# Performance work log

Hardware: AMD Instinct MI355X
Metric: run time of the kernel (lower is better)

## Reference

```python
import jax, jax.numpy as jnp
import numpy as np

L_IMG, L_TXT, B, C, T, D = 12, 12, 64, 1000, 8, 512


def setup_inputs() -> dict:
    key = jax.random.key(0)
    ks = jax.random.split(key, 8)
    s = 0.05  # keep attention logits in a sane range
    return {
        "x": jax.random.normal(ks[0], (L_IMG, B, D), jnp.float32),                 # per-layer projected CLS feats [L,B,D]
        "text_features": jax.random.normal(ks[1], (C, L_TXT, T, D), jnp.float32),  # precomputed per-class text feats
        "self_in_w": jax.random.normal(ks[2], (3 * D, D), jnp.float32) * s,
        "self_in_b": jnp.zeros((3 * D,), jnp.float32),
        "self_out_w": jax.random.normal(ks[3], (D, D), jnp.float32) * s,
        "self_out_b": jnp.zeros((D,), jnp.float32),
        "cross_in_w": jax.random.normal(ks[4], (3 * D, D), jnp.float32) * s,
        "cross_in_b": jnp.zeros((3 * D,), jnp.float32),
        "cross_out_w": jax.random.normal(ks[5], (D, D), jnp.float32) * s,
        "cross_out_b": jnp.zeros((D,), jnp.float32),
        "logit_scale": jnp.full((1,), np.log(1.0 / 0.07), jnp.float32),
    }


def reference(x, text_features, self_in_w, self_in_b, self_out_w, self_out_b,
              cross_in_w, cross_in_b, cross_out_w, cross_out_b, logit_scale):
    d = x.shape[-1]
    scale = 1.0 / jnp.sqrt(jnp.asarray(d, x.dtype))

    # ---- self-attention over the layer axis (torch MHA, 1 head, seq-first [L,B,D]) ----
    Wq, Wk, Wv = jnp.split(self_in_w, 3, axis=0)
    bq, bk, bv = jnp.split(self_in_b, 3, axis=0)
    q = jnp.einsum('lbd,ed->lbe', x, Wq) + bq
    k = jnp.einsum('lbd,ed->lbe', x, Wk) + bk
    v = jnp.einsum('lbd,ed->lbe', x, Wv) + bv
    attn = jax.nn.softmax(jnp.einsum('lbe,mbe->blm', q, k) * scale, axis=-1)
    xs = jnp.einsum('blm,mbe->lbe', attn, v) @ self_out_w.T + self_out_b   # [L,B,D]
    image_features = xs[-1]                                               # [B,D]

    # ---- batched cross-attention: query = image layer-tokens, key/value = per-class,
    #      per-template text layer-tokens; averaged over templates and query layers ----
    cWq, cWk, cWv = jnp.split(cross_in_w, 3, axis=0)
    cbq, cbk, cbv = jnp.split(cross_in_b, 3, axis=0)
    q2 = jnp.einsum('lbd,ed->lbe', xs, cWq) + cbq                          # [L,B,E]
    k2 = jnp.einsum('cmtd,ed->cmte', text_features, cWk) + cbk             # [C,M,T,E]
    v2 = jnp.einsum('cmtd,ed->cmte', text_features, cWv) + cbv
    a2 = jax.nn.softmax(jnp.einsum('lbe,cmte->bctlm', q2, k2) * scale, axis=-1)
    n_avg = a2.shape[2] * a2.shape[3]                                      # T * L_img
    # out_proj is linear, so mean over (template, layer) commutes with it
    ctx = jnp.einsum('bctlm,cmtd->bcd', a2, v2) / n_avg                    # [B,C,D]
    txt = ctx @ cross_out_w.T + cross_out_b                                # [B,C,D]

    # ---- normalize and compute logits (matching the source's permute(1,2,0) + norm(dim=-1)) ----
    tf = jnp.transpose(txt, (0, 2, 1))                                     # [B,D,C]
    img_n = image_features / jnp.linalg.norm(image_features, axis=-1, keepdims=True)
    tf_n = tf / jnp.linalg.norm(tf, axis=-1, keepdims=True)
    return jnp.exp(logit_scale[0]) * jnp.einsum('bd,bdc->bc', img_n, tf_n)  # [B,C]
```

## Files before the change

### kernel.cpp

```cpp
#include <hip/hip_runtime.h>

#define L_IMG 12
#define BATCH 64
#define NCLS  1000
#define DIM   512
#define NTM   96
#define SCALEF 0.044194173824159216f

typedef __attribute__((ext_vector_type(8))) short bf16x8;
typedef __attribute__((ext_vector_type(4))) float f32x4;

__device__ __forceinline__ float bf2f(unsigned short u) {
    return __uint_as_float(((unsigned int)u) << 16);
}
__device__ __forceinline__ unsigned short f2bf(float f) {
    unsigned int u = __float_as_uint(f);
    u += 0x7FFFu + ((u >> 16) & 1u);
    return (unsigned short)(u >> 16);
}
__device__ __forceinline__ void storeo(float* p, float v) { *p = v; }
__device__ __forceinline__ void storeo(unsigned short* p, float v) { *p = f2bf(v); }

__device__ __forceinline__ int swz(int row, int u) {
    return (row << 5) + ((u ^ ((row >> 1) & 3)) << 3);
}

__device__ __forceinline__ void gload16(const unsigned short* g, unsigned short* l) {
    __builtin_amdgcn_global_load_lds(
        (const __attribute__((address_space(1))) void*)g,
        (__attribute__((address_space(3))) void*)l, 16, 0, 0);
}

__global__ __launch_bounds__(256)
void f2bf_kernel(const float* __restrict__ in, unsigned short* __restrict__ out, int n)
{
    int i = (blockIdx.x * 256 + threadIdx.x) * 4;
    if (i < n) {
        float4 v = *(const float4*)(in + i);
        ushort4 o;
        o.x = f2bf(v.x); o.y = f2bf(v.y); o.z = f2bf(v.z); o.w = f2bf(v.w);
        *(ushort4*)(out + i) = o;
    }
}

__global__ __launch_bounds__(256)
void fold_wvo(const float* __restrict__ cow, const float* __restrict__ cWv,
              const float* __restrict__ cbv, unsigned short* __restrict__ Wvob,
              float* __restrict__ bvo)
{
    __shared__ float crow[DIM];
    __shared__ float red[256];
    const int d = blockIdx.x, t = threadIdx.x;
    float c0 = cow[d * DIM + t], c1 = cow[d * DIM + t + 256];
    crow[t] = c0; crow[t + 256] = c1;
    red[t] = c0 * cbv[t] + c1 * cbv[t + 256];
    __syncthreads();
    for (int s = 128; s > 0; s >>= 1) {
        if (t < s) red[t] += red[t + s];
        __syncthreads();
    }
    if (t == 0) bvo[d] = red[0];
    float a0 = 0.f, a1 = 0.f;
    for (int e = 0; e < DIM; e++) {
        float ce = crow[e];
        a0 += ce * cWv[e * DIM + t];
        a1 += ce * cWv[e * DIM + t + 256];
    }
    Wvob[d * DIM + t]       = f2bf(a0);
    Wvob[d * DIM + t + 256] = f2bf(a1);
}

#define BKT 32
#define LDT 68
__global__ __launch_bounds__(256)
void gemm_bt_f32(const float* __restrict__ A, const float* __restrict__ W,
                 const float* __restrict__ bias, float* __restrict__ Co,
                 int M, int N, int K, float out_scale)
{
    __shared__ float As[BKT * LDT];
    __shared__ float Ws[BKT * LDT];
    const int tid = threadIdx.x;
    const int m0 = blockIdx.y << 6, n0 = blockIdx.x << 6;
    const int tx = tid & 15, ty = tid >> 4;
    float acc[4][4] = {};
    for (int k0 = 0; k0 < K; k0 += BKT) {
        #pragma unroll
        for (int i = 0; i < 2; i++) {
            int slot = tid + (i << 8);
            int r = slot >> 3, kq = slot & 7;
            float4 v = *(const float4*)(A + (size_t)(m0 + r) * K + k0 + (kq << 2));
            As[(kq*4+0)*LDT + r] = v.x; As[(kq*4+1)*LDT + r] = v.y;
            As[(kq*4+2)*LDT + r] = v.z; As[(kq*4+3)*LDT + r] = v.w;
            float4 w = *(const float4*)(W + (size_t)(n0 + r) * K + k0 + (kq << 2));
            Ws[(kq*4+0)*LDT + r] = w.x; Ws[(kq*4+1)*LDT + r] = w.y;
            Ws[(kq*4+2)*LDT + r] = w.z; Ws[(kq*4+3)*LDT + r] = w.w;
        }
        __syncthreads();
        #pragma unroll
        for (int kk = 0; kk < BKT; kk++) {
            float4 a = *(const float4*)(As + kk*LDT + ty*4);
            float4 w = *(const float4*)(Ws + kk*LDT + tx*4);
            acc[0][0] += a.x*w.x; acc[0][1] += a.x*w.y; acc[0][2] += a.x*w.z; acc[0][3] += a.x*w.w;
            acc[1][0] += a.y*w.x; acc[1][1] += a.y*w.y; acc[1][2] += a.y*w.z; acc[1][3] += a.y*w.w;
            acc[2][0] += a.z*w.x; acc[2][1] += a.z*w.y; acc[2][2] += a.z*w.z; acc[2][3] += a.z*w.w;
            acc[3][0] += a.w*w.x; acc[3][1] += a.w*w.y; acc[3][2] += a.w*w.z; acc[3][3] += a.w*w.w;
        }
        __syncthreads();
    }
    #pragma unroll
    for (int i = 0; i < 4; i++) {
        int mr = m0 + ty*4 + i;
        #pragma unroll
        for (int j = 0; j < 4; j++) {
            int n = n0 + tx*4 + j;
            float v = acc[i][j];
            if (bias) v += bias[n];
            Co[(size_t)mr * N + n] = v * out_scale;
        }
    }
}

__global__ __launch_bounds__(256)
void gemm_nt_f32(const float* __restrict__ A, const float* __restrict__ W,
                 float* __restrict__ Co, int M, int N, int K)
{
    __shared__ float As[BKT * LDT];
    __shared__ float Ws[BKT * LDT];
    const int tid = threadIdx.x;
    const int m0 = blockIdx.y << 6, n0 = blockIdx.x << 6;
    const int tx = tid & 15, ty = tid >> 4;
    float acc[4][4] = {};
    for (int k0 = 0; k0 < K; k0 += BKT) {
        #pragma unroll
        for (int i = 0; i < 2; i++) {
            int slot = tid + (i << 8);
            int r = slot >> 3, kq = slot & 7;
            float4 v = *(const float4*)(A + (size_t)(m0 + r) * K + k0 + (kq << 2));
            As[(kq*4+0)*LDT + r] = v.x; As[(kq*4+1)*LDT + r] = v.y;
            As[(kq*4+2)*LDT + r] = v.z; As[(kq*4+3)*LDT + r] = v.w;
            int kr = slot >> 4, c4 = slot & 15;
            *(float4*)(Ws + kr*LDT + c4*4) =
                *(const float4*)(W + (size_t)(k0 + kr) * N + n0 + (c4 << 2));
        }
        __syncthreads();
        #pragma unroll
        for (int kk = 0; kk < BKT; kk++) {
            float4 a = *(const float4*)(As + kk*LDT + ty*4);
            float4 w = *(const float4*)(Ws + kk*LDT + tx*4);
            acc[0][0] += a.x*w.x; acc[0][1] += a.x*w.y; acc[0][2] += a.x*w.z; acc[0][3] += a.x*w.w;
            acc[1][0] += a.y*w.x; acc[1][1] += a.y*w.y; acc[1][2] += a.y*w.z; acc[1][3] += a.y*w.w;
            acc[2][0] += a.z*w.x; acc[2][1] += a.z*w.y; acc[2][2] += a.z*w.z; acc[2][3] += a.z*w.w;
            acc[3][0] += a.w*w.x; acc[3][1] += a.w*w.y; acc[3][2] += a.w*w.z; acc[3][3] += a.w*w.w;
        }
        __syncthreads();
    }
    #pragma unroll
    for (int i = 0; i < 4; i++) {
        int mr = m0 + ty*4 + i;
        #pragma unroll
        for (int j = 0; j < 4; j++)
            Co[(size_t)mr * N + n0 + tx*4 + j] = acc[i][j];
    }
}

__global__ __launch_bounds__(256)
void attn_kernel(const float* __restrict__ qkv, float* __restrict__ ao)
{
    __shared__ float lq[L_IMG * DIM];
    __shared__ float lk[L_IMG * DIM];
    __shared__ float sc[L_IMG * L_IMG];
    __shared__ float sa[L_IMG * L_IMG];
    const int b = blockIdx.x, tid = threadIdx.x;
    for (int i = 0; i < 6; i++) {
        int slot = tid + (i << 8);
        int l = slot >> 7, e4 = slot & 127;
        const float* row = qkv + (size_t)(l * BATCH + b) * 1536;
        *(float4*)(lq + l*DIM + e4*4) = *(const float4*)(row + e4*4);
        *(float4*)(lk + l*DIM + e4*4) = *(const float4*)(row + DIM + e4*4);
    }
    __syncthreads();
    if (tid < 144) {
        int l = tid / 12, m = tid % 12;
        float a = 0.f;
        for (int d4 = 0; d4 < 128; d4++) {
            float4 q = *(const float4*)(lq + l*DIM + d4*4);
            float4 k = *(const float4*)(lk + m*DIM + d4*4);
            a += q.x*k.x + q.y*k.y + q.z*k.z + q.w*k.w;
        }
        sc[tid] = a * SCALEF;
    }
    __syncthreads();
    if (tid < 12) {
        float mx = -1e30f;
        for (int m = 0; m < 12; m++) mx = fmaxf(mx, sc[tid*12 + m]);
        float e[12], s = 0.f;
        for (int m = 0; m < 12; m++) { e[m] = __expf(sc[tid*12 + m] - mx); s += e[m]; }
        float inv = 1.f / s;
        for (int m = 0; m < 12; m++) sa[tid*12 + m] = e[m] * inv;
    }
    __syncthreads();
    for (int i = 0; i < 2; i++) {
        int e = tid + (i << 8);
        float vv[12];
        #pragma unroll
        for (int m = 0; m < 12; m++)
            vv[m] = qkv[(size_t)(m * BATCH + b) * 1536 + 1024 + e];
        #pragma unroll
        for (int l = 0; l < 12; l++) {
            float a = 0.f;
            #pragma unroll
            for (int m = 0; m < 12; m++) a += sa[l*12 + m] * vv[m];
            ao[(size_t)(l * BATCH + b) * DIM + e] = a;
        }
    }
}

__global__ __launch_bounds__(256)
void img_kernel(const float* __restrict__ xs, float* __restrict__ imgn)
{
    __shared__ float red[256];
    const int b = blockIdx.x, tid = threadIdx.x;
    const float* row = xs + (size_t)(11 * BATCH + b) * DIM;
    float v0 = row[tid], v1 = row[tid + 256];
    red[tid] = v0*v0 + v1*v1;
    __syncthreads();
    for (int s = 128; s > 0; s >>= 1) {
        if (tid < s) red[tid] += red[tid + s];
        __syncthreads();
    }
    float inv = rsqrtf(red[0]);
    imgn[b*DIM + tid]       = v0 * inv;
    imgn[b*DIM + tid + 256] = v1 * inv;
}

__global__ __launch_bounds__(256)
void build_q2p(const float* __restrict__ q2s, unsigned short* __restrict__ q2pb)
{
    const int l = blockIdx.x, b = blockIdx.y, t = threadIdx.x;
    int d0 = t * 2;
    unsigned int o = 0;
    if (l < 12) {
        float2 v = *(const float2*)(q2s + (size_t)(l * BATCH + b) * DIM + d0);
        o = (unsigned int)f2bf(v.x) | ((unsigned int)f2bf(v.y) << 16);
    }
    ((unsigned int*)q2pb)[(size_t)(b * 16 + l) * 256 + t] = o;
}

template<typename OutT>
__global__ __launch_bounds__(256, 4)
void gemm_mfma(const unsigned short* __restrict__ A, const unsigned short* __restrict__ W,
               const float* __restrict__ bias, OutT* __restrict__ Co,
               int M, int N, float scale)
{
    const int K = DIM;
    __shared__ __align__(16) unsigned short AsBuf[2][128 * 32];
    __shared__ __align__(16) unsigned short WsBuf[2][128 * 32];
    const int m0 = blockIdx.y << 7, n0 = blockIdx.x << 7;
    const int tid = threadIdx.x;
    const int w = tid >> 6, lane = tid & 63;
    const int mt0 = (w & 1) * 4, nt0 = (w >> 1) * 4;
    const int r16 = lane & 15, kq = lane >> 4;
    const int row0 = (w << 5) + (lane >> 2), row1 = row0 + 16;
    const int sc0 = ((lane & 3) ^ ((row0 >> 1) & 3)) << 3;
    const int sc1 = ((lane & 3) ^ ((row1 >> 1) & 3)) << 3;
    const unsigned short* gA0 = A + (size_t)(m0 + row0) * K + sc0;
    const unsigned short* gA1 = A + (size_t)(m0 + row1) * K + sc1;
    const unsigned short* gW0 = W + (size_t)(n0 + row0) * K + sc0;
    const unsigned short* gW1 = W + (size_t)(n0 + row1) * K + sc1;
    const int lw = w << 10;
    int offa[4], offb[4];
    #pragma unroll
    for (int i = 0; i < 4; i++) {
        offa[i] = swz((mt0 + i) * 16 + r16, kq);
        offb[i] = swz((nt0 + i) * 16 + r16, kq);
    }
    f32x4 acc[4][4] = {};

    gload16(gA0, AsBuf[0] + lw);
    gload16(gA1, AsBuf[0] + lw + 512);
    gload16(gW0, WsBuf[0] + lw);
    gload16(gW1, WsBuf[0] + lw + 512);
    __syncthreads();

    #pragma unroll
    for (int t = 0; t < 16; t++) {
        const int cur = t & 1, nxt = cur ^ 1;
        if (t < 15) {
            const int ko = (t + 1) << 5;
            gload16(gA0 + ko, AsBuf[nxt] + lw);
            gload16(gA1 + ko, AsBuf[nxt] + lw + 512);
            gload16(gW0 + ko, WsBuf[nxt] + lw);
            gload16(gW1 + ko, WsBuf[nxt] + lw + 512);
        }
        bf16x8 af[4], bfr[4];
        #pragma unroll
        for (int i = 0; i < 4; i++) {
            af[i]  = *(const bf16x8*)(AsBuf[cur] + offa[i]);
            bfr[i] = *(const bf16x8*)(WsBuf[cur] + offb[i]);
        }
        #pragma unroll
        for (int i = 0; i < 4; i++)
            #pragma unroll
            for (int j = 0; j < 4; j++)
                acc[i][j] = __builtin_amdgcn_mfma_f32_16x16x32_bf16(af[i], bfr[j], acc[i][j], 0, 0, 0);
        if (t < 15) __syncthreads();
    }
    const int rbase = (lane >> 4) * 4;
    #pragma unroll
    for (int i = 0; i < 4; i++)
        #pragma unroll
        for (int j = 0; j < 4; j++) {
            int gcol = n0 + (nt0 + j) * 16 + r16;
            float bv = bias ? bias[gcol] : 0.f;
            #pragma unroll
            for (int r = 0; r < 4; r++) {
                int grow = m0 + (mt0 + i) * 16 + rbase + r;
                storeo(Co + (size_t)grow * N + gcol, acc[i][j][r] * scale + bv);
            }
        }
}

__global__ __launch_bounds__(256, 5)
void fused_scores(const unsigned short* __restrict__ q2pb, const unsigned short* __restrict__ k2,
                  float* __restrict__ wout)
{
    __shared__ __align__(16) unsigned short AsBuf[2][128 * 32];
    __shared__ __align__(16) unsigned short KsBuf[2][96 * 32];
    const int bid = blockIdx.x;
    const int g = bid >> 6, r = bid & 63;
    const int c = g * 8 + (r & 7), bg = r >> 3;
    const int tid = threadIdx.x;
    const int m0 = bg << 7;
    const int w = tid >> 6, lane = tid & 63;
    const int mt0 = w * 2;
    const int r16 = lane & 15, kq = lane >> 4;
    const size_t kb = (size_t)c * NTM * DIM;
    const int row0 = (w << 5) + (lane >> 2), row1 = row0 + 16;
    const int sc0 = ((lane & 3) ^ ((row0 >> 1) & 3)) << 3;
    const int sc1 = ((lane & 3) ^ ((row1 >> 1) & 3)) << 3;
    const unsigned short* gA0 = q2pb + (size_t)(m0 + row0) * DIM + sc0;
    const unsigned short* gA1 = q2pb + (size_t)(m0 + row1) * DIM + sc1;
    const unsigned short* gK0 = k2 + kb + (size_t)row0 * DIM + sc0;
    const unsigned short* gK1 = k2 + kb + (size_t)row1 * DIM + sc1;
    const bool kw = (w < 3);
    const int lw = w << 10;
    int offa[2], offk[6];
    #pragma unroll
    for (int i = 0; i < 2; i++) offa[i] = swz((mt0 + i) * 16 + r16, kq);
    #pragma unroll
    for (int j = 0; j < 6; j++) offk[j] = swz(j * 16 + r16, kq);
    f32x4 acc[2][6] = {};

    gload16(gA0, AsBuf[0] + lw);
    gload16(gA1, AsBuf[0] + lw + 512);
    if (kw) {
        gload16(gK0, KsBuf[0] + lw);
        gload16(gK1, KsBuf[0] + lw + 512);
    }
    __syncthreads();

    #pragma unroll
    for (int t = 0; t < 16; t++) {
        const int cur = t & 1, nxt = cur ^ 1;
        if (t < 15) {
            const int ko = (t + 1) << 5;
            gload16(gA0 + ko, AsBuf[nxt] + lw);
            gload16(gA1 + ko, AsBuf[nxt] + lw + 512);
            if (kw) {
                gload16(gK0 + ko, KsBuf[nxt] + lw);
                gload16(gK1 + ko, KsBuf[nxt] + lw + 512);
            }
        }
        bf16x8 af[2], bfr[6];
        #pragma unroll
        for (int i = 0; i < 2; i++)
            af[i] = *(const bf16x8*)(AsBuf[cur] + offa[i]);
        #pragma unroll
        for (int j = 0; j < 6; j++)
            bfr[j] = *(const bf16x8*)(KsBuf[cur] + offk[j]);
        __builtin_amdgcn_s_setprio(1);
        #pragma unroll
        for (int j = 0; j < 6; j++) {
            acc[0][j] = __builtin_amdgcn_mfma_f32_16x16x32_bf16(af[0], bfr[j], acc[0][j], 0, 0, 0);
            acc[1][j] = __builtin_amdgcn_mfma_f32_16x16x32_bf16(af[1], bfr[j], acc[1][j], 0, 0, 0);
        }
        __builtin_amdgcn_s_setprio(0);
        if (t < 15) __syncthreads();
    }

    #pragma unroll
    for (int i = 0; i < 2; i++) {
        #pragma unroll
        for (int rr = 0; rr < 4; rr++) {
            float v0 = acc[i][0][rr], v1 = acc[i][1][rr], v2 = acc[i][2][rr];
            float v3 = acc[i][3][rr], v4 = acc[i][4][rr], v5 = acc[i][5][rr];
            float mx = fmaxf(fmaxf(fmaxf(v0, v1), fmaxf(v2, v3)), fmaxf(v4, v5));
            mx = fmaxf(mx, __shfl_xor(mx, 8, 64));
            float e0 = __expf(v0 - mx), e1 = __expf(v1 - mx), e2 = __expf(v2 - mx);
            float e3 = __expf(v3 - mx), e4 = __expf(v4 - mx), e5 = __expf(v5 - mx);
            float s = e0 + e1 + e2 + e3 + e4 + e5;
            s += __shfl_xor(s, 8, 64);
            float inv = 1.f / (96.f * s);
            acc[i][0][rr] = e0 * inv; acc[i][1][rr] = e1 * inv; acc[i][2][rr] = e2 * inv;
            acc[i][3][rr] = e3 * inv; acc[i][4][rr] = e4 * inv; acc[i][5][rr] = e5 * inv;
        }
    }

    const bool contrib = (lane >> 4) < 3;
    #pragma unroll
    for (int i = 0; i < 2; i++) {
        float s6[6];
        #pragma unroll
        for (int j = 0; j < 6; j++) {
            float t = contrib ? (acc[i][j][0] + acc[i][j][1] + acc[i][j][2] + acc[i][j][3]) : 0.f;
            t += __shfl_xor(t, 16, 64);
            t += __shfl_xor(t, 32, 64);
            s6[j] = t;
        }
        if (lane < 16) {
            const int b = bg * 8 + mt0 + i;
            float* dst = wout + ((size_t)(b * NCLS + c)) * NTM;
            #pragma unroll
            for (int j = 0; j < 6; j++)
                dst[j * 16 + r16] = s6[j];
        }
    }
}

__global__ __launch_bounds__(256)
void txt_kernel(const float* __restrict__ wbuf, const unsigned short* __restrict__ v2p,
                const float* __restrict__ cob, unsigned short* __restrict__ txt)
{
    __shared__ float ws[16 * NTM];
    const int c = blockIdx.x, bg = blockIdx.y, tid = threadIdx.x;
    for (int idx = tid; idx < 16 * NTM; idx += 256) {
        int bl = idx / NTM, tm = idx - bl * NTM;
        ws[idx] = wbuf[((size_t)((bg * 16 + bl) * NCLS + c)) * NTM + tm];
    }
    __syncthreads();
    float a0[16] = {}, a1[16] = {};
    const unsigned int* vrow = (const unsigned int*)(v2p + (size_t)c * NTM * DIM) + tid;
    for (int tm = 0; tm < NTM; tm++) {
        unsigned int u = vrow[tm * 256];
        float vx = __uint_as_float(u << 16);
        float vy = __uint_as_float(u & 0xFFFF0000u);
        #pragma unroll
        for (int bl = 0; bl < 16; bl++) {
            float wv = ws[bl * NTM + tm];
            a0[bl] += wv * vx; a1[bl] += wv * vy;
        }
    }
    int d0 = tid * 2;
    float c0 = cob[d0], c1 = cob[d0 + 1];
    #pragma unroll
    for (int bl = 0; bl < 16; bl++) {
        int b = bg * 16 + bl;
        unsigned int o = (unsigned int)f2bf(a0[bl] + c0) | ((unsigned int)f2bf(a1[bl] + c1) << 16);
        ((unsigned int*)txt)[(size_t)(b * NCLS + c) * 256 + tid] = o;
    }
}

__global__ __launch_bounds__(256)
void n2_kernel(const unsigned short* __restrict__ txt, float* __restrict__ n2)
{
    const int b = blockIdx.x, cg = blockIdx.y, t = threadIdx.x;
    float a0 = 0.f, a1 = 0.f;
    const unsigned int* p = (const unsigned int*)txt + ((size_t)(b * NCLS + cg * 125)) * 256 + t;
    for (int c = 0; c < 125; c++) {
        unsigned int u = p[c * 256];
        float vx = __uint_as_float(u << 16);
        float vy = __uint_as_float(u & 0xFFFF0000u);
        a0 += vx * vx; a1 += vy * vy;
    }
    atomicAdd(&n2[b * DIM + t * 2], a0);
    atomicAdd(&n2[b * DIM + t * 2 + 1], a1);
}

__global__ __launch_bounds__(256)
void u_kernel(const float* __restrict__ imgn, const float* __restrict__ n2,
              const float* __restrict__ logit_scale, float* __restrict__ u)
{
    int i = blockIdx.x * 256 + threadIdx.x;
    float els = expf(logit_scale[0]);
    u[i] = els * imgn[i] * rsqrtf(n2[i]);
}

__global__ __launch_bounds__(256)
void logits_kernel(const unsigned short* __restrict__ txt, const float* __restrict__ u,
                   float* __restrict__ out)
{
    __shared__ float lu[DIM];
    const int b = blockIdx.y, cg = blockIdx.x, tid = threadIdx.x;
    lu[tid]       = u[b*DIM + tid];
    lu[tid + 256] = u[b*DIM + tid + 256];
    __syncthreads();
    int wave = tid >> 6, lane = tid & 63;
    int c = (cg << 2) + wave;
    const unsigned short* row = txt + (size_t)(b * NCLS + c) * DIM;
    ushort4 p0 = ((const ushort4*)row)[lane*2];
    ushort4 p1 = ((const ushort4*)row)[lane*2 + 1];
    int d0 = lane * 8;
    float s = bf2f(p0.x)*lu[d0]   + bf2f(p0.y)*lu[d0+1] + bf2f(p0.z)*lu[d0+2] + bf2f(p0.w)*lu[d0+3]
            + bf2f(p1.x)*lu[d0+4] + bf2f(p1.y)*lu[d0+5] + bf2f(p1.z)*lu[d0+6] + bf2f(p1.w)*lu[d0+7];
    #pragma unroll
    for (int off = 32; off > 0; off >>= 1) s += __shfl_down(s, off, 64);
    if (lane == 0) out[b*NCLS + c] = s;
}

extern "C" void kernel_launch(void* const* d_in, const int* in_sizes, int n_in,
                              void* d_out, int out_size, void* d_ws, size_t ws_size,
                              hipStream_t stream)
{
    const float* x   = (const float*)d_in[0];
    const float* tfe = (const float*)d_in[1];
    const float* siw = (const float*)d_in[2];
    const float* sib = (const float*)d_in[3];
    const float* sow = (const float*)d_in[4];
    const float* sob = (const float*)d_in[5];
    const float* ciw = (const float*)d_in[6];
    const float* cib = (const float*)d_in[7];
    const float* cow = (const float*)d_in[8];
    const float* cob = (const float*)d_in[9];
    const float* ls  = (const float*)d_in[10];
    float* out = (float*)d_out;

    char* p = (char*)d_ws;
    auto alloc = [&](size_t bytes) { char* r = p; p += (bytes + 255) & ~255ull; return r; };
    unsigned short* tfeb = (unsigned short*)alloc((size_t)49152000 * 2);
    unsigned short* v2p  = (unsigned short*)alloc((size_t)96000 * DIM * 2);
    float* wbuf          = (float*)alloc((size_t)BATCH * NCLS * NTM * 4);
    float* qkv           = (float*)alloc((size_t)768 * 1536 * 4);
    float* ao            = (float*)alloc((size_t)768 * DIM * 4);
    float* xs            = (float*)alloc((size_t)768 * DIM * 4);
    float* q2s           = (float*)alloc((size_t)768 * DIM * 4);
    float* q2k           = (float*)alloc((size_t)768 * DIM * 4);
    unsigned short* q2pb = (unsigned short*)alloc((size_t)1024 * DIM * 2);
    unsigned short* Wvob = (unsigned short*)alloc((size_t)DIM * DIM * 2);
    float* bvo           = (float*)alloc(DIM * 4);
    float* n2            = (float*)alloc(BATCH * DIM * 4);
    float* uu            = (float*)alloc(BATCH * DIM * 4);
    float* imgn          = (float*)alloc(BATCH * DIM * 4);
    unsigned short* txt  = tfeb;

    hipMemsetAsync(n2, 0, BATCH * DIM * 4, stream);

    f2bf_kernel<<<48000, 256, 0, stream>>>(tfe, tfeb, 49152000);
    fold_wvo<<<512, 256, 0, stream>>>(cow, ciw + 1024*512, cib + 1024, Wvob, bvo);

    gemm_bt_f32<<<dim3(24, 12), 256, 0, stream>>>(x, siw, sib, qkv, 768, 1536, 512, 1.f);
    attn_kernel<<<64, 256, 0, stream>>>(qkv, ao);
    gemm_bt_f32<<<dim3(8, 12), 256, 0, stream>>>(ao, sow, sob, xs, 768, 512, 512, 1.f);
    img_kernel<<<64, 256, 0, stream>>>(xs, imgn);
    gemm_bt_f32<<<dim3(8, 12), 256, 0, stream>>>(xs, ciw, cib, q2s, 768, 512, 512, SCALEF);
    gemm_nt_f32<<<dim3(8, 12), 256, 0, stream>>>(q2s, ciw + 512*512, q2k, 768, 512, 512);
    build_q2p<<<dim3(16, 64), 256, 0, stream>>>(q2k, q2pb);

    gemm_mfma<unsigned short><<<dim3(4, 750), 256, 0, stream>>>(
        tfeb, Wvob, bvo, v2p, 96000, 512, 1.f);

    fused_scores<<<8000, 256, 0, stream>>>(q2pb, tfeb, wbuf);

    txt_kernel<<<dim3(1000, 4), 256, 0, stream>>>(wbuf, v2p, cob, txt);
    n2_kernel<<<dim3(64, 8), 256, 0, stream>>>(txt, n2);
    u_kernel<<<128, 256, 0, stream>>>(imgn, n2, ls, uu);
    logits_kernel<<<dim3(250, 64), 256, 0, stream>>>(txt, uu, out);
}
```

Measured before the change: 816.6 us.

## Apply folded value/output projection after attention-weighted reduction instead of before

Reorders the cross-attention value path: the attention-weighted sum over text tokens now runs on the raw bf16 text features, and the folded Wv·Wout projection (with the combined bias) is applied afterwards as a 64000-row MFMA GEMM instead of a 96000-row one. This cuts GEMM rows and drops the v2p intermediate. It also fuses u_kernel into logits_kernel and swizzles the ctx_kernel block order so classes are grouped. The tradeoff is an extra bf16 rounding of the context before projection, and the bias is now added once after the sum, which is only exact if the attention weights sum to the averaging constant.

```diff
diff --git a/kernel.cpp b/kernel.cpp
--- a/kernel.cpp
+++ b/kernel.cpp
@@ -45,8 +45,8 @@
 
 __global__ __launch_bounds__(256)
 void fold_wvo(const float* __restrict__ cow, const float* __restrict__ cWv,
-              const float* __restrict__ cbv, unsigned short* __restrict__ Wvob,
-              float* __restrict__ bvo)
+              const float* __restrict__ cbv, const float* __restrict__ cob,
+              unsigned short* __restrict__ Wvob, float* __restrict__ bvo)
 {
     __shared__ float crow[DIM];
     __shared__ float red[256];
@@ -59,7 +59,7 @@
         if (t < s) red[t] += red[t + s];
         __syncthreads();
     }
-    if (t == 0) bvo[d] = red[0];
+    if (t == 0) bvo[d] = red[0] + cob[d];
     float a0 = 0.f, a1 = 0.f;
     for (int e = 0; e < DIM; e++) {
         float ce = crow[e];
@@ -428,18 +428,21 @@
 }
 
 __global__ __launch_bounds__(256)
-void txt_kernel(const float* __restrict__ wbuf, const unsigned short* __restrict__ v2p,
-                const float* __restrict__ cob, unsigned short* __restrict__ txt)
+void ctx_kernel(const float* __restrict__ wbuf, const unsigned short* __restrict__ tfeb,
+                unsigned short* __restrict__ ctxraw)
 {
     __shared__ float ws[16 * NTM];
-    const int c = blockIdx.x, bg = blockIdx.y, tid = threadIdx.x;
+    const int bid = blockIdx.x;
+    const int g = bid >> 5, r = bid & 31;
+    const int c = g * 8 + (r & 7), bg = r >> 3;
+    const int tid = threadIdx.x;
     for (int idx = tid; idx < 16 * NTM; idx += 256) {
         int bl = idx / NTM, tm = idx - bl * NTM;
         ws[idx] = wbuf[((size_t)((bg * 16 + bl) * NCLS + c)) * NTM + tm];
     }
     __syncthreads();
     float a0[16] = {}, a1[16] = {};
-    const unsigned int* vrow = (const unsigned int*)(v2p + (size_t)c * NTM * DIM) + tid;
+    const unsigned int* vrow = (const unsigned int*)(tfeb + (size_t)c * NTM * DIM) + tid;
     for (int tm = 0; tm < NTM; tm++) {
         unsigned int u = vrow[tm * 256];
         float vx = __uint_as_float(u << 16);
@@ -450,13 +453,11 @@
             a0[bl] += wv * vx; a1[bl] += wv * vy;
         }
     }
-    int d0 = tid * 2;
-    float c0 = cob[d0], c1 = cob[d0 + 1];
     #pragma unroll
     for (int bl = 0; bl < 16; bl++) {
         int b = bg * 16 + bl;
-        unsigned int o = (unsigned int)f2bf(a0[bl] + c0) | ((unsigned int)f2bf(a1[bl] + c1) << 16);
-        ((unsigned int*)txt)[(size_t)(b * NCLS + c) * 256 + tid] = o;
+        unsigned int o = (unsigned int)f2bf(a0[bl]) | ((unsigned int)f2bf(a1[bl]) << 16);
+        ((unsigned int*)ctxraw)[(size_t)(b * NCLS + c) * 256 + tid] = o;
     }
 }
 
@@ -477,22 +478,15 @@
 }
 
 __global__ __launch_bounds__(256)
-void u_kernel(const float* __restrict__ imgn, const float* __restrict__ n2,
-              const float* __restrict__ logit_scale, float* __restrict__ u)
-{
-    int i = blockIdx.x * 256 + threadIdx.x;
-    float els = expf(logit_scale[0]);
-    u[i] = els * imgn[i] * rsqrtf(n2[i]);
-}
-
-__global__ __launch_bounds__(256)
-void logits_kernel(const unsigned short* __restrict__ txt, const float* __restrict__ u,
+void logits_kernel(const unsigned short* __restrict__ txt, const float* __restrict__ imgn,
+                   const float* __restrict__ n2, const float* __restrict__ logit_scale,
                    float* __restrict__ out)
 {
     __shared__ float lu[DIM];
     const int b = blockIdx.y, cg = blockIdx.x, tid = threadIdx.x;
-    lu[tid]       = u[b*DIM + tid];
-    lu[tid + 256] = u[b*DIM + tid + 256];
+    float els = expf(logit_scale[0]);
+    lu[tid]       = els * imgn[b*DIM + tid]       * rsqrtf(n2[b*DIM + tid]);
+    lu[tid + 256] = els * imgn[b*DIM + tid + 256] * rsqrtf(n2[b*DIM + tid + 256]);
     __syncthreads();
     int wave = tid >> 6, lane = tid & 63;
     int c = (cg << 2) + wave;
@@ -526,26 +520,25 @@
 
     char* p = (char*)d_ws;
     auto alloc = [&](size_t bytes) { char* r = p; p += (bytes + 255) & ~255ull; return r; };
-    unsigned short* tfeb = (unsigned short*)alloc((size_t)49152000 * 2);
-    unsigned short* v2p  = (unsigned short*)alloc((size_t)96000 * DIM * 2);
-    float* wbuf          = (float*)alloc((size_t)BATCH * NCLS * NTM * 4);
-    float* qkv           = (float*)alloc((size_t)768 * 1536 * 4);
-    float* ao            = (float*)alloc((size_t)768 * DIM * 4);
-    float* xs            = (float*)alloc((size_t)768 * DIM * 4);
-    float* q2s           = (float*)alloc((size_t)768 * DIM * 4);
-    float* q2k           = (float*)alloc((size_t)768 * DIM * 4);
-    unsigned short* q2pb = (unsigned short*)alloc((size_t)1024 * DIM * 2);
-    unsigned short* Wvob = (unsigned short*)alloc((size_t)DIM * DIM * 2);
-    float* bvo           = (float*)alloc(DIM * 4);
-    float* n2            = (float*)alloc(BATCH * DIM * 4);
-    float* uu            = (float*)alloc(BATCH * DIM * 4);
-    float* imgn          = (float*)alloc(BATCH * DIM * 4);
-    unsigned short* txt  = tfeb;
+    unsigned short* tfeb   = (unsigned short*)alloc((size_t)49152000 * 2);
+    unsigned short* ctxraw = (unsigned short*)alloc((size_t)BATCH * NCLS * DIM * 2);
+    float* wbuf            = (float*)alloc((size_t)BATCH * NCLS * NTM * 4);
+    float* qkv             = (float*)alloc((size_t)768 * 1536 * 4);
+    float* ao              = (float*)alloc((size_t)768 * DIM * 4);
+    float* xs              = (float*)alloc((size_t)768 * DIM * 4);
+    float* q2s             = (float*)alloc((size_t)768 * DIM * 4);
+    float* q2k             = (float*)alloc((size_t)768 * DIM * 4);
+    unsigned short* q2pb   = (unsigned short*)alloc((size_t)1024 * DIM * 2);
+    unsigned short* Wvob   = (unsigned short*)alloc((size_t)DIM * DIM * 2);
+    float* bvo             = (float*)alloc(DIM * 4);
+    float* n2              = (float*)alloc(BATCH * DIM * 4);
+    float* imgn            = (float*)alloc(BATCH * DIM * 4);
+    unsigned short* txt    = tfeb;
 
     hipMemsetAsync(n2, 0, BATCH * DIM * 4, stream);
 
     f2bf_kernel<<<48000, 256, 0, stream>>>(tfe, tfeb, 49152000);
-    fold_wvo<<<512, 256, 0, stream>>>(cow, ciw + 1024*512, cib + 1024, Wvob, bvo);
+    fold_wvo<<<512, 256, 0, stream>>>(cow, ciw + 1024*512, cib + 1024, cob, Wvob, bvo);
 
     gemm_bt_f32<<<dim3(24, 12), 256, 0, stream>>>(x, siw, sib, qkv, 768, 1536, 512, 1.f);
     attn_kernel<<<64, 256, 0, stream>>>(qkv, ao);
@@ -555,13 +548,13 @@
     gemm_nt_f32<<<dim3(8, 12), 256, 0, stream>>>(q2s, ciw + 512*512, q2k, 768, 512, 512);
     build_q2p<<<dim3(16, 64), 256, 0, stream>>>(q2k, q2pb);
 
-    gemm_mfma<unsigned short><<<dim3(4, 750), 256, 0, stream>>>(
-        tfeb, Wvob, bvo, v2p, 96000, 512, 1.f);
-
     fused_scores<<<8000, 256, 0, stream>>>(q2pb, tfeb, wbuf);
 
-    txt_kernel<<<dim3(1000, 4), 256, 0, stream>>>(wbuf, v2p, cob, txt);
+    ctx_kernel<<<4000, 256, 0, stream>>>(wbuf, tfeb, ctxraw);
+
+    gemm_mfma<unsigned short><<<dim3(4, 500), 256, 0, stream>>>(
+        ctxraw, Wvob, bvo, txt, 64000, 512, 1.f);
+
     n2_kernel<<<dim3(64, 8), 256, 0, stream>>>(txt, n2);
-    u_kernel<<<128, 256, 0, stream>>>(imgn, n2, ls, uu);
-    logits_kernel<<<dim3(250, 64), 256, 0, stream>>>(txt, uu, out);
-}
+    logits_kernel<<<dim3(250, 64), 256, 0, stream>>>(txt, imgn, n2, ls, out);
+}
```

After: 793.1 us. 2.9% less time.
